# Performance work log

Hardware: AMD Instinct MI355X
Metric: run time of the kernel (lower is better)

## Reference

```python
import jax, jax.numpy as jnp
import numpy as np

ALPHA = 0.2   # LeakyReLU negative slope
RATIO = 0.5   # blend ratio between attention and structural similarity
KHOP = 3      # k-hop structural similarity depth
NEG_BIG = -9e15


def _build_adj(edge, n):
    # edge: [N, D] int neighbor indices; adj[i, edge[i, d]] = 1
    rows = jnp.broadcast_to(jnp.arange(n)[:, None], edge.shape)
    return jnp.zeros((n, n), jnp.float32).at[rows, edge].set(1.0)


def _structural_similarity(adj, khop):
    # Sum of adjacency powers A + A^2 + ... + A^khop (k-hop reachability counts).
    s = adj
    p = adj
    for _ in range(khop - 1):
        p = p @ adj
        s = s + p
    return s


def _per_graph(atom, edge, W, a):
    n = atom.shape[0]
    adj = _build_adj(edge, n)
    structure = jax.nn.softmax(_structural_similarity(adj, KHOP), axis=1)
    h = atom @ W                                   # [N, F]
    f = h.shape[1]
    # a_input[i,j] = concat(h_i, h_j); a_input @ a == (h @ a1)_i + (h @ a2)_j
    src = h @ a[:f, 0]                             # [N]
    dst = h @ a[f:, 0]                             # [N]
    e = jax.nn.leaky_relu(src[:, None] + dst[None, :], ALPHA)  # [N, N]
    att = jnp.where(adj > 0, e, NEG_BIG)
    att = jax.nn.softmax(att, axis=1)
    blended = RATIO * att + (1.0 - RATIO) * structure
    return jax.nn.elu(blended @ h)                 # [N, F]


def setup_inputs() -> dict:
    key = jax.random.key(0)
    k1, k2, k3, k4 = jax.random.split(key, 4)
    B, N, D, F_IN, F_OUT = 16, 1024, 8, 128, 64
    atoms = jax.random.normal(k1, (B, N, F_IN), dtype=jnp.float32)
    edges = jax.random.randint(k2, (B, N, D), 0, N, dtype=jnp.int64)
    W = jax.random.normal(k3, (F_IN, F_OUT), dtype=jnp.float32) * 0.1
    a = jax.random.normal(k4, (2 * F_OUT, 1), dtype=jnp.float32) * 0.1
    return {"atoms": atoms, "edges": edges, "W": W, "a": a}


def reference(atoms, edges, W, a):
    return jax.vmap(_per_graph, in_axes=(0, 0, None, None))(atoms, edges, W, a)
```

## Files before the change

kernel.cpp:

```cpp
#include <hip/hip_runtime.h>

#define NN 1024
#define DG 8
#define FO 64
#define FI 128
#define LALPHA 0.2f
#define BR 16
#define SBS 257
#define RDS 68

typedef __attribute__((ext_vector_type(8))) short bf16x8;
typedef __attribute__((ext_vector_type(4))) float f32x4;

static __device__ __forceinline__ unsigned short f2bf(float x) {
  union { float f; unsigned u; } v; v.f = x;
  unsigned r = v.u + 0x7FFFu + ((v.u >> 16) & 1u);
  return (unsigned short)(r >> 16);
}
static __device__ __forceinline__ float bf2f(unsigned short h) {
  union { unsigned u; float f; } v; v.u = ((unsigned)h) << 16;
  return v.f;
}

__global__ __launch_bounds__(256) void k_prep(const float* __restrict__ atoms,
                                              const float* __restrict__ W,
                                              const float* __restrict__ a,
                                              const int* __restrict__ edges,
                                              int* __restrict__ uniq,
                                              ushort* __restrict__ hT,
                                              ushort* __restrict__ hN,
                                              float* __restrict__ srcv,
                                              float* __restrict__ dstv) {
  __shared__ float sp[16], dp[16];
  const int t = threadIdx.x, b = blockIdx.x;
  const int g = b >> 6;
  const int rbase = b * 16;

  if (t < 16) {
    sp[t] = 0.f; dp[t] = 0.f;
    const int rr = rbase + t;
    int e[DG];
#pragma unroll
    for (int s = 0; s < DG; s++) e[s] = edges[rr * DG + s];
#pragma unroll
    for (int s = 0; s < DG; s++) {
      int v = e[s];
      bool dup = false;
#pragma unroll
      for (int q = 0; q < DG; q++)
        if (q < s && e[q] == v) dup = true;
      uniq[rr * DG + s] = dup ? -1 : v;
    }
  }

  const int w = t >> 6, lane = t & 63, quad = lane >> 4, l16 = lane & 15;
  const float* __restrict__ Ar = atoms + (size_t)(rbase + l16) * FI;
  const float* __restrict__ Wc = W + w * 16 + l16;
  f32x4 acc = {0.f, 0.f, 0.f, 0.f};
#pragma unroll
  for (int kc = 0; kc < 4; kc++) {
    const int k0 = kc * 32 + quad * 8;
    float4 a0 = *(const float4*)(Ar + k0);
    float4 a1 = *(const float4*)(Ar + k0 + 4);
    float av[8] = {a0.x, a0.y, a0.z, a0.w, a1.x, a1.y, a1.z, a1.w};
    float wv[8];
#pragma unroll
    for (int e = 0; e < 8; e++) wv[e] = Wc[(k0 + e) * FO];
    bf16x8 ahi, alo, bhi, blo;
#pragma unroll
    for (int e = 0; e < 8; e++) {
      ushort h = f2bf(av[e]);
      ahi[e] = (short)h;
      alo[e] = (short)f2bf(av[e] - bf2f(h));
      ushort g2 = f2bf(wv[e]);
      bhi[e] = (short)g2;
      blo[e] = (short)f2bf(wv[e] - bf2f(g2));
    }
    acc = __builtin_amdgcn_mfma_f32_16x16x32_bf16(ahi, bhi, acc, 0, 0, 0);
    acc = __builtin_amdgcn_mfma_f32_16x16x32_bf16(ahi, blo, acc, 0, 0, 0);
    acc = __builtin_amdgcn_mfma_f32_16x16x32_bf16(alo, bhi, acc, 0, 0, 0);
  }

  const int f = w * 16 + l16;
  const float as_ = a[f], ad_ = a[FO + f];
  float ps[4], pd[4];
#pragma unroll
  for (int r = 0; r < 4; r++) {
    float v = acc[r];
    int rb = rbase + quad * 4 + r;
    ushort hv = f2bf(v);
    hT[((size_t)g * FO + f) * NN + (rb & (NN - 1))] = hv;
    hN[(size_t)rb * FO + f] = hv;
    ps[r] = v * as_;
    pd[r] = v * ad_;
  }
#pragma unroll
  for (int off = 1; off < 16; off <<= 1)
#pragma unroll
    for (int r = 0; r < 4; r++) {
      ps[r] += __shfl_xor(ps[r], off);
      pd[r] += __shfl_xor(pd[r], off);
    }
  __syncthreads();
  if (l16 == 0) {
#pragma unroll
    for (int r = 0; r < 4; r++) {
      atomicAdd(&sp[quad * 4 + r], ps[r]);
      atomicAdd(&dp[quad * 4 + r], pd[r]);
    }
  }
  __syncthreads();
  if (t < 16) {
    srcv[rbase + t] = sp[t];
    dstv[rbase + t] = dp[t];
  }
}

__global__ __launch_bounds__(256, 4) void k_fused(const int* __restrict__ uniq,
                                                  const float* __restrict__ srcv,
                                                  const float* __restrict__ dstv,
                                                  const ushort* __restrict__ hT,
                                                  const ushort* __restrict__ hN,
                                                  float* __restrict__ out) {
  __shared__ unsigned Sb[BR * SBS];
  __shared__ __align__(16) float red[4][BR][RDS];
  __shared__ float zred[4][16];
  __shared__ int n1[BR][DG];
  __shared__ float attw[BR][DG];

  const int t = threadIdx.x, b = blockIdx.x;
  const int g = b >> 6, rbase = (b & 63) * BR;
  const int* __restrict__ Ug = uniq + (size_t)g * NN * DG;

  for (int i = t; i < BR * SBS; i += 256) Sb[i] = 0u;
  if (t < BR * DG) n1[t >> 3][t & 7] = Ug[(rbase + (t >> 3)) * DG + (t & 7)];
  __syncthreads();

#pragma unroll
  for (int q = 0; q < 4; q++) {
    int idx = t + 256 * q;
    int r = idx & 15, e = idx >> 4;
    int j = n1[r][e >> 3];
    if (j >= 0) {
      if ((e & 7) == 0)
        atomicAdd(&Sb[r * SBS + (j >> 2)], 1u << ((j & 3) * 8));
      int k = Ug[j * DG + (e & 7)];
      if (k >= 0) {
        atomicAdd(&Sb[r * SBS + (k >> 2)], 1u << ((k & 3) * 8));
        int4 m0 = *(const int4*)(Ug + k * DG);
        int4 m1 = *(const int4*)(Ug + k * DG + 4);
        int ll[8] = {m0.x, m0.y, m0.z, m0.w, m1.x, m1.y, m1.z, m1.w};
#pragma unroll
        for (int e2 = 0; e2 < 8; e2++)
          if (ll[e2] >= 0) atomicAdd(&Sb[r * SBS + (ll[e2] >> 2)], 1u << ((ll[e2] & 3) * 8));
      }
    }
  }
  if (t < BR) {
    int r = t;
    float si = srcv[g * NN + rbase + r];
    float ev[DG];
    float m = -1e30f;
#pragma unroll
    for (int s = 0; s < DG; s++) {
      int j = n1[r][s];
      if (j >= 0) {
        float x = si + dstv[g * NN + j];
        x = x > 0.f ? x : LALPHA * x;
        ev[s] = x;
        m = fmaxf(m, x);
      } else ev[s] = -1e30f;
    }
    float sm = 0.f;
#pragma unroll
    for (int s = 0; s < DG; s++) {
      float e = (n1[r][s] >= 0) ? __expf(ev[s] - m) : 0.f;
      ev[s] = e;
      sm += e;
    }
    float inv = 1.f / sm;
#pragma unroll
    for (int s = 0; s < DG; s++) attw[r][s] = ev[s] * inv;
  }
  __syncthreads();

  const int rr_ = t >> 4, f0_ = (t & 15) * 4;
  float ah0 = 0.f, ah1 = 0.f, ah2 = 0.f, ah3 = 0.f;
#pragma unroll
  for (int s = 0; s < DG; s++) {
    int j = n1[rr_][s];
    if (j >= 0) {
      float wgt = attw[rr_][s];
      uint2 hv = *(const uint2*)(hN + ((size_t)(g * NN + j)) * FO + f0_);
      ah0 += wgt * bf2f((ushort)(hv.x & 0xffffu));
      ah1 += wgt * bf2f((ushort)(hv.x >> 16));
      ah2 += wgt * bf2f((ushort)(hv.y & 0xffffu));
      ah3 += wgt * bf2f((ushort)(hv.y >> 16));
    }
  }

  const int v = t >> 6, lane = t & 63, quad = lane >> 4, l16 = lane & 15;
  const int k0 = v * 256;
  const ushort* __restrict__ hb = hT + ((size_t)g * FO) * NN;
  f32x4 acc[4] = {{0.f, 0.f, 0.f, 0.f}, {0.f, 0.f, 0.f, 0.f},
                  {0.f, 0.f, 0.f, 0.f}, {0.f, 0.f, 0.f, 0.f}};
  float zacc = 0.f;
#pragma unroll
  for (int ks = 0; ks < 256; ks += 32) {
    const int wd = l16 * SBS + ((k0 + ks) >> 2) + quad * 2;
    unsigned s0 = Sb[wd], s1 = Sb[wd + 1];
    const int c0 = s0 & 255u, c1 = (s0 >> 8) & 255u, c2 = (s0 >> 16) & 255u, c3 = s0 >> 24;
    const int c4 = s1 & 255u, c5 = (s1 >> 8) & 255u, c6 = (s1 >> 16) & 255u, c7 = s1 >> 24;
    const float e0 = __expf((float)c0), e1 = __expf((float)c1);
    const float e2 = __expf((float)c2), e3 = __expf((float)c3);
    const float e4 = __expf((float)c4), e5 = __expf((float)c5);
    const float e6 = __expf((float)c6), e7 = __expf((float)c7);
    bf16x8 af;
    af[0] = (short)f2bf(e0); af[1] = (short)f2bf(e1);
    af[2] = (short)f2bf(e2); af[3] = (short)f2bf(e3);
    af[4] = (short)f2bf(e4); af[5] = (short)f2bf(e5);
    af[6] = (short)f2bf(e6); af[7] = (short)f2bf(e7);
    zacc += (e0 + e1) + (e2 + e3) + (e4 + e5) + (e6 + e7);
    const ushort* hp = hb + (size_t)l16 * NN + k0 + ks + quad * 8;
#pragma unroll
    for (int ct = 0; ct < 4; ct++) {
      bf16x8 bf = *(const bf16x8*)(hp + (size_t)(ct * 16) * NN);
      acc[ct] = __builtin_amdgcn_mfma_f32_16x16x32_bf16(af, bf, acc[ct], 0, 0, 0);
    }
  }
  zacc += __shfl_xor(zacc, 16);
  zacc += __shfl_xor(zacc, 32);
  if (lane < 16) zred[v][lane] = zacc;
#pragma unroll
  for (int ct = 0; ct < 4; ct++)
#pragma unroll
    for (int r = 0; r < 4; r++)
      red[v][quad * 4 + r][ct * 16 + l16] = acc[ct][r];
  __syncthreads();

  const float Z = zred[0][rr_] + zred[1][rr_] + zred[2][rr_] + zred[3][rr_];
  const float hz = 0.5f / Z;
  f32x4 s = *(const f32x4*)&red[0][rr_][f0_];
  f32x4 s1v = *(const f32x4*)&red[1][rr_][f0_];
  f32x4 s2v = *(const f32x4*)&red[2][rr_][f0_];
  f32x4 s3v = *(const f32x4*)&red[3][rr_][f0_];
  float o0 = 0.5f * ah0 + (s[0] + s1v[0] + s2v[0] + s3v[0]) * hz;
  float o1 = 0.5f * ah1 + (s[1] + s1v[1] + s2v[1] + s3v[1]) * hz;
  float o2 = 0.5f * ah2 + (s[2] + s1v[2] + s2v[2] + s3v[2]) * hz;
  float o3 = 0.5f * ah3 + (s[3] + s1v[3] + s2v[3] + s3v[3]) * hz;
  o0 = o0 > 0.f ? o0 : __expf(o0) - 1.f;
  o1 = o1 > 0.f ? o1 : __expf(o1) - 1.f;
  o2 = o2 > 0.f ? o2 : __expf(o2) - 1.f;
  o3 = o3 > 0.f ? o3 : __expf(o3) - 1.f;
  *(float4*)(out + ((size_t)(g * NN + rbase + rr_)) * FO + f0_) =
      make_float4(o0, o1, o2, o3);
}

extern "C" void kernel_launch(void* const* d_in, const int* in_sizes, int n_in,
                              void* d_out, int out_size, void* d_ws, size_t ws_size,
                              hipStream_t stream) {
  const float* atoms = (const float*)d_in[0];
  const int* edges = (const int*)d_in[1];
  const float* W = (const float*)d_in[2];
  const float* a = (const float*)d_in[3];
  float* out = (float*)d_out;

  const int nrows = in_sizes[0] / FI;
  const int ngraph = nrows / NN;

  ushort* hT = (ushort*)d_ws;
  ushort* hN = hT + (size_t)ngraph * FO * NN;
  float* srcv = (float*)(hN + (size_t)nrows * FO);
  float* dstv = srcv + nrows;
  int* uniq = (int*)(dstv + nrows);

  k_prep<<<nrows / 16, 256, 0, stream>>>(atoms, W, a, edges, uniq, hT, hN, srcv, dstv);
  k_fused<<<ngraph * (NN / BR), 256, 0, stream>>>(uniq, srcv, dstv, hT, hN, out);
}
```

Baseline: 96.66 us.

## Split fused kernel across feature halves and alias reduction buffer onto count table

Each block now handles 16 rows and only 32 of the 64 output features, which doubles the grid to 128 blocks per graph. The reduction buffer reuses the shared-memory count table after a barrier, and launch bounds rise to 8 blocks per CU. Together these cut shared memory and registers per block to raise occupancy and parallelism. In exchange, the 3-hop structural count build and its exp/bf16 conversion now run twice per row block, so that work is duplicated.

Result: slower. 99.10 us (+2.5%).

```diff
diff --git a/kernel.cpp b/kernel.cpp
--- a/kernel.cpp
+++ b/kernel.cpp
@@ -7,7 +7,7 @@
 #define LALPHA 0.2f
 #define BR 16
 #define SBS 257
-#define RDS 68
+#define RDS2 36
 
 typedef __attribute__((ext_vector_type(8))) short bf16x8;
 typedef __attribute__((ext_vector_type(4))) float f32x4;
@@ -116,23 +116,24 @@
   }
 }
 
-__global__ __launch_bounds__(256, 4) void k_fused(const int* __restrict__ uniq,
+__global__ __launch_bounds__(256, 8) void k_fused(const int* __restrict__ uniq,
                                                   const float* __restrict__ srcv,
                                                   const float* __restrict__ dstv,
                                                   const ushort* __restrict__ hT,
                                                   const ushort* __restrict__ hN,
                                                   float* __restrict__ out) {
-  __shared__ unsigned Sb[BR * SBS];
-  __shared__ __align__(16) float red[4][BR][RDS];
+  __shared__ __align__(16) unsigned SbU[BR * SBS];
   __shared__ float zred[4][16];
   __shared__ int n1[BR][DG];
   __shared__ float attw[BR][DG];
 
   const int t = threadIdx.x, b = blockIdx.x;
-  const int g = b >> 6, rbase = (b & 63) * BR;
+  const int g = b >> 7, bl = b & 127;
+  const int rbase = (bl >> 1) * BR, fh = bl & 1;
   const int* __restrict__ Ug = uniq + (size_t)g * NN * DG;
-
-  for (int i = t; i < BR * SBS; i += 256) Sb[i] = 0u;
+  float* __restrict__ redp = (float*)SbU;
+
+  for (int i = t; i < BR * SBS; i += 256) SbU[i] = 0u;
   if (t < BR * DG) n1[t >> 3][t & 7] = Ug[(rbase + (t >> 3)) * DG + (t & 7)];
   __syncthreads();
 
@@ -143,16 +144,16 @@
     int j = n1[r][e >> 3];
     if (j >= 0) {
       if ((e & 7) == 0)
-        atomicAdd(&Sb[r * SBS + (j >> 2)], 1u << ((j & 3) * 8));
+        atomicAdd(&SbU[r * SBS + (j >> 2)], 1u << ((j & 3) * 8));
       int k = Ug[j * DG + (e & 7)];
       if (k >= 0) {
-        atomicAdd(&Sb[r * SBS + (k >> 2)], 1u << ((k & 3) * 8));
+        atomicAdd(&SbU[r * SBS + (k >> 2)], 1u << ((k & 3) * 8));
         int4 m0 = *(const int4*)(Ug + k * DG);
         int4 m1 = *(const int4*)(Ug + k * DG + 4);
         int ll[8] = {m0.x, m0.y, m0.z, m0.w, m1.x, m1.y, m1.z, m1.w};
 #pragma unroll
         for (int e2 = 0; e2 < 8; e2++)
-          if (ll[e2] >= 0) atomicAdd(&Sb[r * SBS + (ll[e2] >> 2)], 1u << ((ll[e2] & 3) * 8));
+          if (ll[e2] >= 0) atomicAdd(&SbU[r * SBS + (ll[e2] >> 2)], 1u << ((ll[e2] & 3) * 8));
       }
     }
   }
@@ -184,31 +185,34 @@
   }
   __syncthreads();
 
-  const int rr_ = t >> 4, f0_ = (t & 15) * 4;
+  const int rr_ = t >> 3, f0l = (t & 7) * 4;
+  const int fgl = fh * 32 + f0l;
   float ah0 = 0.f, ah1 = 0.f, ah2 = 0.f, ah3 = 0.f;
-#pragma unroll
-  for (int s = 0; s < DG; s++) {
-    int j = n1[rr_][s];
-    if (j >= 0) {
-      float wgt = attw[rr_][s];
-      uint2 hv = *(const uint2*)(hN + ((size_t)(g * NN + j)) * FO + f0_);
-      ah0 += wgt * bf2f((ushort)(hv.x & 0xffffu));
-      ah1 += wgt * bf2f((ushort)(hv.x >> 16));
-      ah2 += wgt * bf2f((ushort)(hv.y & 0xffffu));
-      ah3 += wgt * bf2f((ushort)(hv.y >> 16));
+  if (t < BR * 8) {
+#pragma unroll
+    for (int s = 0; s < DG; s++) {
+      int j = n1[rr_][s];
+      if (j >= 0) {
+        float wgt = attw[rr_][s];
+        uint2 hv = *(const uint2*)(hN + ((size_t)(g * NN + j)) * FO + fgl);
+        ah0 += wgt * bf2f((ushort)(hv.x & 0xffffu));
+        ah1 += wgt * bf2f((ushort)(hv.x >> 16));
+        ah2 += wgt * bf2f((ushort)(hv.y & 0xffffu));
+        ah3 += wgt * bf2f((ushort)(hv.y >> 16));
+      }
     }
   }
 
   const int v = t >> 6, lane = t & 63, quad = lane >> 4, l16 = lane & 15;
   const int k0 = v * 256;
   const ushort* __restrict__ hb = hT + ((size_t)g * FO) * NN;
-  f32x4 acc[4] = {{0.f, 0.f, 0.f, 0.f}, {0.f, 0.f, 0.f, 0.f},
-                  {0.f, 0.f, 0.f, 0.f}, {0.f, 0.f, 0.f, 0.f}};
+  const size_t cof = (size_t)(fh * 32) * NN;
+  f32x4 acc0 = {0.f, 0.f, 0.f, 0.f}, acc1 = {0.f, 0.f, 0.f, 0.f};
   float zacc = 0.f;
 #pragma unroll
   for (int ks = 0; ks < 256; ks += 32) {
     const int wd = l16 * SBS + ((k0 + ks) >> 2) + quad * 2;
-    unsigned s0 = Sb[wd], s1 = Sb[wd + 1];
+    unsigned s0 = SbU[wd], s1 = SbU[wd + 1];
     const int c0 = s0 & 255u, c1 = (s0 >> 8) & 255u, c2 = (s0 >> 16) & 255u, c3 = s0 >> 24;
     const int c4 = s1 & 255u, c5 = (s1 >> 8) & 255u, c6 = (s1 >> 16) & 255u, c7 = s1 >> 24;
     const float e0 = __expf((float)c0), e1 = __expf((float)c1);
@@ -222,38 +226,42 @@
     af[6] = (short)f2bf(e6); af[7] = (short)f2bf(e7);
     zacc += (e0 + e1) + (e2 + e3) + (e4 + e5) + (e6 + e7);
     const ushort* hp = hb + (size_t)l16 * NN + k0 + ks + quad * 8;
-#pragma unroll
-    for (int ct = 0; ct < 4; ct++) {
-      bf16x8 bf = *(const bf16x8*)(hp + (size_t)(ct * 16) * NN);
-      acc[ct] = __builtin_amdgcn_mfma_f32_16x16x32_bf16(af, bf, acc[ct], 0, 0, 0);
-    }
+    bf16x8 bA = *(const bf16x8*)(hp + cof);
+    bf16x8 bB = *(const bf16x8*)(hp + cof + (size_t)16 * NN);
+    acc0 = __builtin_amdgcn_mfma_f32_16x16x32_bf16(af, bA, acc0, 0, 0, 0);
+    acc1 = __builtin_amdgcn_mfma_f32_16x16x32_bf16(af, bB, acc1, 0, 0, 0);
   }
   zacc += __shfl_xor(zacc, 16);
   zacc += __shfl_xor(zacc, 32);
+
+  __syncthreads();
+
   if (lane < 16) zred[v][lane] = zacc;
 #pragma unroll
-  for (int ct = 0; ct < 4; ct++)
-#pragma unroll
-    for (int r = 0; r < 4; r++)
-      red[v][quad * 4 + r][ct * 16 + l16] = acc[ct][r];
-  __syncthreads();
-
-  const float Z = zred[0][rr_] + zred[1][rr_] + zred[2][rr_] + zred[3][rr_];
-  const float hz = 0.5f / Z;
-  f32x4 s = *(const f32x4*)&red[0][rr_][f0_];
-  f32x4 s1v = *(const f32x4*)&red[1][rr_][f0_];
-  f32x4 s2v = *(const f32x4*)&red[2][rr_][f0_];
-  f32x4 s3v = *(const f32x4*)&red[3][rr_][f0_];
-  float o0 = 0.5f * ah0 + (s[0] + s1v[0] + s2v[0] + s3v[0]) * hz;
-  float o1 = 0.5f * ah1 + (s[1] + s1v[1] + s2v[1] + s3v[1]) * hz;
-  float o2 = 0.5f * ah2 + (s[2] + s1v[2] + s2v[2] + s3v[2]) * hz;
-  float o3 = 0.5f * ah3 + (s[3] + s1v[3] + s2v[3] + s3v[3]) * hz;
-  o0 = o0 > 0.f ? o0 : __expf(o0) - 1.f;
-  o1 = o1 > 0.f ? o1 : __expf(o1) - 1.f;
-  o2 = o2 > 0.f ? o2 : __expf(o2) - 1.f;
-  o3 = o3 > 0.f ? o3 : __expf(o3) - 1.f;
-  *(float4*)(out + ((size_t)(g * NN + rbase + rr_)) * FO + f0_) =
-      make_float4(o0, o1, o2, o3);
+  for (int r = 0; r < 4; r++) {
+    redp[((v * 16) + quad * 4 + r) * RDS2 + 0 * 16 + l16] = acc0[r];
+    redp[((v * 16) + quad * 4 + r) * RDS2 + 1 * 16 + l16] = acc1[r];
+  }
+  __syncthreads();
+
+  if (t < BR * 8) {
+    const float Z = zred[0][rr_] + zred[1][rr_] + zred[2][rr_] + zred[3][rr_];
+    const float hz = 0.5f / Z;
+    f32x4 s = *(const f32x4*)&redp[(0 * 16 + rr_) * RDS2 + f0l];
+    f32x4 s1v = *(const f32x4*)&redp[(1 * 16 + rr_) * RDS2 + f0l];
+    f32x4 s2v = *(const f32x4*)&redp[(2 * 16 + rr_) * RDS2 + f0l];
+    f32x4 s3v = *(const f32x4*)&redp[(3 * 16 + rr_) * RDS2 + f0l];
+    float o0 = 0.5f * ah0 + (s[0] + s1v[0] + s2v[0] + s3v[0]) * hz;
+    float o1 = 0.5f * ah1 + (s[1] + s1v[1] + s2v[1] + s3v[1]) * hz;
+    float o2 = 0.5f * ah2 + (s[2] + s1v[2] + s2v[2] + s3v[2]) * hz;
+    float o3 = 0.5f * ah3 + (s[3] + s1v[3] + s2v[3] + s3v[3]) * hz;
+    o0 = o0 > 0.f ? o0 : __expf(o0) - 1.f;
+    o1 = o1 > 0.f ? o1 : __expf(o1) - 1.f;
+    o2 = o2 > 0.f ? o2 : __expf(o2) - 1.f;
+    o3 = o3 > 0.f ? o3 : __expf(o3) - 1.f;
+    *(float4*)(out + ((size_t)(g * NN + rbase + rr_)) * FO + fgl) =
+        make_float4(o0, o1, o2, o3);
+  }
 }
 
 extern "C" void kernel_launch(void* const* d_in, const int* in_sizes, int n_in,
@@ -275,5 +283,5 @@
   int* uniq = (int*)(dstv + nrows);
 
   k_prep<<<nrows / 16, 256, 0, stream>>>(atoms, W, a, edges, uniq, hT, hN, srcv, dstv);
-  k_fused<<<ngraph * (NN / BR), 256, 0, stream>>>(uniq, srcv, dstv, hT, hN, out);
-}
+  k_fused<<<ngraph * 128, 256, 0, stream>>>(uniq, srcv, dstv, hT, hN, out);
+}
```

## Process 32 rows per block, reusing each hT fragment for two MFMA tiles

Applied to the files above, without the earlier changes.

Doubles the rows handled per block from 16 to 32. Each bf16 fragment of hT loaded from global memory now feeds two MFMA accumulator sets, which halves hT traffic per output row. The structural-count buffer Sb is aliased onto the reduction buffer so shared memory stays bounded. In exchange, the grid has half as many blocks, register pressure is higher, and the launch bound drops to 2 blocks per CU, which lowers occupancy and latency hiding. It also relies on the hidden launch code and k_prep staying consistent with the new BR value.

New measurement: 97.65 us. No clear change (+1.0%).

```diff
diff --git a/kernel.cpp b/kernel.cpp
--- a/kernel.cpp
+++ b/kernel.cpp
@@ -5,7 +5,7 @@
 #define FO 64
 #define FI 128
 #define LALPHA 0.2f
-#define BR 16
+#define BR 32
 #define SBS 257
 #define RDS 68
 
@@ -116,30 +116,30 @@
   }
 }
 
-__global__ __launch_bounds__(256, 4) void k_fused(const int* __restrict__ uniq,
+__global__ __launch_bounds__(256, 2) void k_fused(const int* __restrict__ uniq,
                                                   const float* __restrict__ srcv,
                                                   const float* __restrict__ dstv,
                                                   const ushort* __restrict__ hT,
                                                   const ushort* __restrict__ hN,
                                                   float* __restrict__ out) {
-  __shared__ unsigned Sb[BR * SBS];
-  __shared__ __align__(16) float red[4][BR][RDS];
-  __shared__ float zred[4][16];
+  __shared__ __align__(16) float redU[4 * BR * RDS];
+  __shared__ float zred[4][BR];
   __shared__ int n1[BR][DG];
   __shared__ float attw[BR][DG];
+  unsigned* __restrict__ Sb = (unsigned*)redU;
 
   const int t = threadIdx.x, b = blockIdx.x;
-  const int g = b >> 6, rbase = (b & 63) * BR;
+  const int g = b >> 5, rbase = (b & 31) * BR;
   const int* __restrict__ Ug = uniq + (size_t)g * NN * DG;
 
   for (int i = t; i < BR * SBS; i += 256) Sb[i] = 0u;
-  if (t < BR * DG) n1[t >> 3][t & 7] = Ug[(rbase + (t >> 3)) * DG + (t & 7)];
-  __syncthreads();
-
-#pragma unroll
-  for (int q = 0; q < 4; q++) {
+  n1[t >> 3][t & 7] = Ug[(rbase + (t >> 3)) * DG + (t & 7)];
+  __syncthreads();
+
+#pragma unroll
+  for (int q = 0; q < 8; q++) {
     int idx = t + 256 * q;
-    int r = idx & 15, e = idx >> 4;
+    int r = idx & 31, e = idx >> 5;
     int j = n1[r][e >> 3];
     if (j >= 0) {
       if ((e & 7) == 0)
@@ -184,76 +184,137 @@
   }
   __syncthreads();
 
-  const int rr_ = t >> 4, f0_ = (t & 15) * 4;
-  float ah0 = 0.f, ah1 = 0.f, ah2 = 0.f, ah3 = 0.f;
+  const int rA = t >> 4, rB = rA + 16, f0_ = (t & 15) * 4;
+  float aA0 = 0.f, aA1 = 0.f, aA2 = 0.f, aA3 = 0.f;
+  float aB0 = 0.f, aB1 = 0.f, aB2 = 0.f, aB3 = 0.f;
 #pragma unroll
   for (int s = 0; s < DG; s++) {
-    int j = n1[rr_][s];
+    int j = n1[rA][s];
     if (j >= 0) {
-      float wgt = attw[rr_][s];
+      float wgt = attw[rA][s];
       uint2 hv = *(const uint2*)(hN + ((size_t)(g * NN + j)) * FO + f0_);
-      ah0 += wgt * bf2f((ushort)(hv.x & 0xffffu));
-      ah1 += wgt * bf2f((ushort)(hv.x >> 16));
-      ah2 += wgt * bf2f((ushort)(hv.y & 0xffffu));
-      ah3 += wgt * bf2f((ushort)(hv.y >> 16));
+      aA0 += wgt * bf2f((ushort)(hv.x & 0xffffu));
+      aA1 += wgt * bf2f((ushort)(hv.x >> 16));
+      aA2 += wgt * bf2f((ushort)(hv.y & 0xffffu));
+      aA3 += wgt * bf2f((ushort)(hv.y >> 16));
+    }
+  }
+#pragma unroll
+  for (int s = 0; s < DG; s++) {
+    int j = n1[rB][s];
+    if (j >= 0) {
+      float wgt = attw[rB][s];
+      uint2 hv = *(const uint2*)(hN + ((size_t)(g * NN + j)) * FO + f0_);
+      aB0 += wgt * bf2f((ushort)(hv.x & 0xffffu));
+      aB1 += wgt * bf2f((ushort)(hv.x >> 16));
+      aB2 += wgt * bf2f((ushort)(hv.y & 0xffffu));
+      aB3 += wgt * bf2f((ushort)(hv.y >> 16));
     }
   }
 
   const int v = t >> 6, lane = t & 63, quad = lane >> 4, l16 = lane & 15;
   const int k0 = v * 256;
   const ushort* __restrict__ hb = hT + ((size_t)g * FO) * NN;
-  f32x4 acc[4] = {{0.f, 0.f, 0.f, 0.f}, {0.f, 0.f, 0.f, 0.f},
-                  {0.f, 0.f, 0.f, 0.f}, {0.f, 0.f, 0.f, 0.f}};
-  float zacc = 0.f;
+  f32x4 accA[4] = {{0.f, 0.f, 0.f, 0.f}, {0.f, 0.f, 0.f, 0.f},
+                   {0.f, 0.f, 0.f, 0.f}, {0.f, 0.f, 0.f, 0.f}};
+  f32x4 accB[4] = {{0.f, 0.f, 0.f, 0.f}, {0.f, 0.f, 0.f, 0.f},
+                   {0.f, 0.f, 0.f, 0.f}, {0.f, 0.f, 0.f, 0.f}};
+  float zaccA = 0.f, zaccB = 0.f;
 #pragma unroll
   for (int ks = 0; ks < 256; ks += 32) {
-    const int wd = l16 * SBS + ((k0 + ks) >> 2) + quad * 2;
-    unsigned s0 = Sb[wd], s1 = Sb[wd + 1];
-    const int c0 = s0 & 255u, c1 = (s0 >> 8) & 255u, c2 = (s0 >> 16) & 255u, c3 = s0 >> 24;
-    const int c4 = s1 & 255u, c5 = (s1 >> 8) & 255u, c6 = (s1 >> 16) & 255u, c7 = s1 >> 24;
-    const float e0 = __expf((float)c0), e1 = __expf((float)c1);
-    const float e2 = __expf((float)c2), e3 = __expf((float)c3);
-    const float e4 = __expf((float)c4), e5 = __expf((float)c5);
-    const float e6 = __expf((float)c6), e7 = __expf((float)c7);
-    bf16x8 af;
-    af[0] = (short)f2bf(e0); af[1] = (short)f2bf(e1);
-    af[2] = (short)f2bf(e2); af[3] = (short)f2bf(e3);
-    af[4] = (short)f2bf(e4); af[5] = (short)f2bf(e5);
-    af[6] = (short)f2bf(e6); af[7] = (short)f2bf(e7);
-    zacc += (e0 + e1) + (e2 + e3) + (e4 + e5) + (e6 + e7);
-    const ushort* hp = hb + (size_t)l16 * NN + k0 + ks + quad * 8;
-#pragma unroll
-    for (int ct = 0; ct < 4; ct++) {
-      bf16x8 bf = *(const bf16x8*)(hp + (size_t)(ct * 16) * NN);
-      acc[ct] = __builtin_amdgcn_mfma_f32_16x16x32_bf16(af, bf, acc[ct], 0, 0, 0);
-    }
-  }
-  zacc += __shfl_xor(zacc, 16);
-  zacc += __shfl_xor(zacc, 32);
-  if (lane < 16) zred[v][lane] = zacc;
+    const int wof = ((k0 + ks) >> 2) + quad * 2;
+    unsigned sA0 = Sb[l16 * SBS + wof], sA1 = Sb[l16 * SBS + wof + 1];
+    unsigned sB0 = Sb[(l16 + 16) * SBS + wof], sB1 = Sb[(l16 + 16) * SBS + wof + 1];
+    {
+      const int c0 = sA0 & 255u, c1 = (sA0 >> 8) & 255u, c2 = (sA0 >> 16) & 255u, c3 = sA0 >> 24;
+      const int c4 = sA1 & 255u, c5 = (sA1 >> 8) & 255u, c6 = (sA1 >> 16) & 255u, c7 = sA1 >> 24;
+      const float e0 = __expf((float)c0), e1 = __expf((float)c1);
+      const float e2 = __expf((float)c2), e3 = __expf((float)c3);
+      const float e4 = __expf((float)c4), e5 = __expf((float)c5);
+      const float e6 = __expf((float)c6), e7 = __expf((float)c7);
+      bf16x8 afA;
+      afA[0] = (short)f2bf(e0); afA[1] = (short)f2bf(e1);
+      afA[2] = (short)f2bf(e2); afA[3] = (short)f2bf(e3);
+      afA[4] = (short)f2bf(e4); afA[5] = (short)f2bf(e5);
+      afA[6] = (short)f2bf(e6); afA[7] = (short)f2bf(e7);
+      zaccA += (e0 + e1) + (e2 + e3) + (e4 + e5) + (e6 + e7);
+      const int c8 = sB0 & 255u, c9 = (sB0 >> 8) & 255u, ca = (sB0 >> 16) & 255u, cb = sB0 >> 24;
+      const int cc = sB1 & 255u, cd = (sB1 >> 8) & 255u, ce = (sB1 >> 16) & 255u, cf = sB1 >> 24;
+      const float f0 = __expf((float)c8), f1 = __expf((float)c9);
+      const float f2 = __expf((float)ca), f3 = __expf((float)cb);
+      const float f4 = __expf((float)cc), f5 = __expf((float)cd);
+      const float f6 = __expf((float)ce), f7 = __expf((float)cf);
+      bf16x8 afB;
+      afB[0] = (short)f2bf(f0); afB[1] = (short)f2bf(f1);
+      afB[2] = (short)f2bf(f2); afB[3] = (short)f2bf(f3);
+      afB[4] = (short)f2bf(f4); afB[5] = (short)f2bf(f5);
+      afB[6] = (short)f2bf(f6); afB[7] = (short)f2bf(f7);
+      zaccB += (f0 + f1) + (f2 + f3) + (f4 + f5) + (f6 + f7);
+      const ushort* hp = hb + (size_t)l16 * NN + k0 + ks + quad * 8;
+#pragma unroll
+      for (int ct = 0; ct < 4; ct++) {
+        bf16x8 bf = *(const bf16x8*)(hp + (size_t)(ct * 16) * NN);
+        accA[ct] = __builtin_amdgcn_mfma_f32_16x16x32_bf16(afA, bf, accA[ct], 0, 0, 0);
+        accB[ct] = __builtin_amdgcn_mfma_f32_16x16x32_bf16(afB, bf, accB[ct], 0, 0, 0);
+      }
+    }
+  }
+  zaccA += __shfl_xor(zaccA, 16);
+  zaccA += __shfl_xor(zaccA, 32);
+  zaccB += __shfl_xor(zaccB, 16);
+  zaccB += __shfl_xor(zaccB, 32);
+
+  __syncthreads();
+
+  if (lane < 16) {
+    zred[v][l16] = zaccA;
+    zred[v][l16 + 16] = zaccB;
+  }
 #pragma unroll
   for (int ct = 0; ct < 4; ct++)
 #pragma unroll
-    for (int r = 0; r < 4; r++)
-      red[v][quad * 4 + r][ct * 16 + l16] = acc[ct][r];
-  __syncthreads();
-
-  const float Z = zred[0][rr_] + zred[1][rr_] + zred[2][rr_] + zred[3][rr_];
-  const float hz = 0.5f / Z;
-  f32x4 s = *(const f32x4*)&red[0][rr_][f0_];
-  f32x4 s1v = *(const f32x4*)&red[1][rr_][f0_];
-  f32x4 s2v = *(const f32x4*)&red[2][rr_][f0_];
-  f32x4 s3v = *(const f32x4*)&red[3][rr_][f0_];
-  float o0 = 0.5f * ah0 + (s[0] + s1v[0] + s2v[0] + s3v[0]) * hz;
-  float o1 = 0.5f * ah1 + (s[1] + s1v[1] + s2v[1] + s3v[1]) * hz;
-  float o2 = 0.5f * ah2 + (s[2] + s1v[2] + s2v[2] + s3v[2]) * hz;
-  float o3 = 0.5f * ah3 + (s[3] + s1v[3] + s2v[3] + s3v[3]) * hz;
-  o0 = o0 > 0.f ? o0 : __expf(o0) - 1.f;
-  o1 = o1 > 0.f ? o1 : __expf(o1) - 1.f;
-  o2 = o2 > 0.f ? o2 : __expf(o2) - 1.f;
-  o3 = o3 > 0.f ? o3 : __expf(o3) - 1.f;
-  *(float4*)(out + ((size_t)(g * NN + rbase + rr_)) * FO + f0_) =
-      make_float4(o0, o1, o2, o3);
+    for (int r = 0; r < 4; r++) {
+      redU[((size_t)v * BR + quad * 4 + r) * RDS + ct * 16 + l16] = accA[ct][r];
+      redU[((size_t)v * BR + 16 + quad * 4 + r) * RDS + ct * 16 + l16] = accB[ct][r];
+    }
+  __syncthreads();
+
+  {
+    const float ZA = zred[0][rA] + zred[1][rA] + zred[2][rA] + zred[3][rA];
+    const float hzA = 0.5f / ZA;
+    f32x4 s = *(const f32x4*)&redU[((size_t)0 * BR + rA) * RDS + f0_];
+    f32x4 s1v = *(const f32x4*)&redU[((size_t)1 * BR + rA) * RDS + f0_];
+    f32x4 s2v = *(const f32x4*)&redU[((size_t)2 * BR + rA) * RDS + f0_];
+    f32x4 s3v = *(const f32x4*)&redU[((size_t)3 * BR + rA) * RDS + f0_];
+    float o0 = 0.5f * aA0 + (s[0] + s1v[0] + s2v[0] + s3v[0]) * hzA;
+    float o1 = 0.5f * aA1 + (s[1] + s1v[1] + s2v[1] + s3v[1]) * hzA;
+    float o2 = 0.5f * aA2 + (s[2] + s1v[2] + s2v[2] + s3v[2]) * hzA;
+    float o3 = 0.5f * aA3 + (s[3] + s1v[3] + s2v[3] + s3v[3]) * hzA;
+    o0 = o0 > 0.f ? o0 : __expf(o0) - 1.f;
+    o1 = o1 > 0.f ? o1 : __expf(o1) - 1.f;
+    o2 = o2 > 0.f ? o2 : __expf(o2) - 1.f;
+    o3 = o3 > 0.f ? o3 : __expf(o3) - 1.f;
+    *(float4*)(out + ((size_t)(g * NN + rbase + rA)) * FO + f0_) =
+        make_float4(o0, o1, o2, o3);
+  }
+  {
+    const float ZB = zred[0][rB] + zred[1][rB] + zred[2][rB] + zred[3][rB];
+    const float hzB = 0.5f / ZB;
+    f32x4 s = *(const f32x4*)&redU[((size_t)0 * BR + rB) * RDS + f0_];
+    f32x4 s1v = *(const f32x4*)&redU[((size_t)1 * BR + rB) * RDS + f0_];
+    f32x4 s2v = *(const f32x4*)&redU[((size_t)2 * BR + rB) * RDS + f0_];
+    f32x4 s3v = *(const f32x4*)&redU[((size_t)3 * BR + rB) * RDS + f0_];
+    float o0 = 0.5f * aB0 + (s[0] + s1v[0] + s2v[0] + s3v[0]) * hzB;
+    float o1 = 0.5f * aB1 + (s[1] + s1v[1] + s2v[1] + s3v[1]) * hzB;
+    float o2 = 0.5f * aB2 + (s[2] + s1v[2] + s2v[2] + s3v[2]) * hzB;
+    float o3 = 0.5f * aB3 + (s[3] + s1v[3] + s2v[3] + s3v[3]) * hzB;
+    o0 = o0 > 0.f ? o0 : __expf(o0) - 1.f;
+    o1 = o1 > 0.f ? o1 : __expf(o1) - 1.f;
+    o2 = o2 > 0.f ? o2 : __expf(o2) - 1.f;
+    o3 = o3 > 0.f ? o3 : __expf(o3) - 1.f;
+    *(float4*)(out + ((size_t)(g * NN + rbase + rB)) * FO + f0_) =
+        make_float4(o0, o1, o2, o3);
+  }
 }
 
 extern "C" void kernel_launch(void* const* d_in, const int* in_sizes, int n_in,
```
